# Kernel optimization log

Hardware: AMD Instinct MI355X
Metric: run time of the kernel (lower is better)

Reference implementation:

```python
import jax, jax.numpy as jnp
import numpy as np

B, C = 8, 2048          # batch, out_dim (projection channels)
HG = WG = 32            # global crop feature map
HL = WL = 12            # local crop feature map
STUDENT_TEMP = 0.1
TEMP_SCHEDULE = np.concatenate([np.linspace(0.04, 0.07, 30), np.ones(100 - 30) * 0.07])

# Fixed relative boxes (x1, x2, y1, y2) per (iq, v) crop pair, shared across the
# batch so grid shapes are static. Source computes grid_H from teacher_feat.shape[0]
# (= C, a quirk of the original code) and grid_W from shape[1] (= spatial H); boxes
# are chosen so resulting grids are ~[22-25, 22-24].
PAIRS = [
    (0, 1, (-0.80, 0.70, -0.500, -0.475), (-0.90, 0.60, -0.60, 0.60)),
    (0, 2, (-0.75, 0.75,  0.100,  0.125), (-0.80, 0.80, -0.80, 0.80)),
    (0, 3, (-0.60, 0.90, -0.200, -0.178), (-0.70, 0.90, -0.90, 0.70)),
    (1, 0, (-0.70, 0.80,  0.300,  0.322), (-0.85, 0.65, -0.50, 0.90)),
    (1, 2, (-0.90, 0.50, -0.100, -0.076), (-0.60, 0.95, -0.95, 0.60)),
    (1, 3, (-0.50, 0.95,  0.200,  0.224), (-0.90, 0.90, -0.40, 0.95)),
]


def _grid_dims(box, Hc, Wc):
    x1, x2, y1, y2 = box
    return int(abs(y1 - y2) / 2 * Hc), int(abs(x1 - x2) / 2 * Wc)  # (grid_H, grid_W)


def _make_grid(box, gH, gW):
    # Faithful to source: meshgrid([linspace(y1,y2,gH), linspace(x1,x2,gW)]),
    # stacked so channel 0 holds the y-linspace (which grid_sample reads as x).
    x1, x2, y1, y2 = box
    yy, xx = jnp.meshgrid(jnp.linspace(y1, y2, gH), jnp.linspace(x1, x2, gW), indexing='ij')
    return jnp.stack([yy, xx], axis=-1)  # [gH, gW, 2]


def _grid_sample_border(img, grid):
    # torch.nn.functional.grid_sample, bilinear, padding_mode='border',
    # align_corners=False. img: [B, C, H, W], grid: [gH, gW, 2] (same grid per batch).
    H, W = img.shape[-2], img.shape[-1]
    gx, gy = grid[..., 0], grid[..., 1]
    ix = jnp.clip((gx + 1.0) * (W * 0.5) - 0.5, 0.0, W - 1.0)  # border: clip coords
    iy = jnp.clip((gy + 1.0) * (H * 0.5) - 0.5, 0.0, H - 1.0)
    x0f, y0f = jnp.floor(ix), jnp.floor(iy)
    wx = (ix - x0f)[None, None]  # [1,1,gH,gW]
    wy = (iy - y0f)[None, None]
    x0 = x0f.astype(jnp.int32)
    y0 = y0f.astype(jnp.int32)
    x1 = jnp.minimum(x0 + 1, W - 1)
    y1 = jnp.minimum(y0 + 1, H - 1)
    v00 = img[:, :, y0, x0]
    v01 = img[:, :, y0, x1]
    v10 = img[:, :, y1, x0]
    v11 = img[:, :, y1, x1]
    return (1.0 - wy) * ((1.0 - wx) * v00 + wx * v01) + wy * ((1.0 - wx) * v10 + wx * v11)


def setup_inputs() -> dict:
    key = jax.random.key(0)
    ks = jax.random.split(key, 7)
    return {
        'student_g0': jax.random.normal(ks[0], (B, C, HG, WG), jnp.float32),
        'student_g1': jax.random.normal(ks[1], (B, C, HG, WG), jnp.float32),
        'student_l0': jax.random.normal(ks[2], (B, C, HL, WL), jnp.float32),
        'student_l1': jax.random.normal(ks[3], (B, C, HL, WL), jnp.float32),
        'teacher_g0': jax.random.normal(ks[4], (B, C, HG, WG), jnp.float32),
        'teacher_g1': jax.random.normal(ks[5], (B, C, HG, WG), jnp.float32),
        'center': jax.random.normal(ks[6], (1, C), jnp.float32) * 0.1,
        'epoch': 5,
    }


def reference(student_g0, student_g1, student_l0, student_l1,
              teacher_g0, teacher_g1, center, epoch):
    temp = float(TEMP_SCHEDULE[epoch])
    students = [s / STUDENT_TEMP for s in (student_g0, student_g1, student_l0, student_l1)]
    cen = center[:, :, None, None]  # [1,C,1,1]
    cteach = [jax.nn.softmax((t - cen) / temp, axis=1) for t in (teacher_g0, teacher_g1)]

    losses = []
    for iq, v, tbox, sbox in PAIRS:
        tfeat = cteach[iq]   # [B,C,H,W]
        sfeat = students[v]  # [B,C,h,w]
        # Faithful: source passes (shape[0]=C, shape[1]=spatial H) as (H, W).
        gH, gW = _grid_dims(tbox, C, tfeat.shape[2])
        t_common = jax.lax.stop_gradient(_grid_sample_border(tfeat, _make_grid(tbox, gH, gW)))
        s_common = _grid_sample_border(sfeat, _make_grid(sbox, gH, gW))
        # cross-entropy over channels -> [B, gH, gW]
        loss = (-t_common * jax.nn.log_softmax(s_common, axis=1)).sum(axis=1)
        losses.append(loss.reshape(-1))
    return jnp.concatenate(losses).mean()
```

## Files before the change

kernel.cpp:

```cpp
#include <hip/hip_runtime.h>
#include <hip/hip_fp16.h>

#define NPOS 26688

struct PairInfo {
  int iq, v, Hs, gH, gW, base, per;
  unsigned magicPer, magicW;
  int tOfs, tN, tCb;
  int sN, sCb;
  float tx1, tx2, ty1, ty2;
  float sx1, sx2, sy1, sy2;
};

__constant__ PairInfo g_pairs[6] = {
  {0,1,32,25,24,    0,600, 7158279u,178956971u,    0,2, 7, 22,5, -0.80f,0.70f,-0.500f,-0.475f,  -0.90f,0.60f,-0.60f,0.60f},
  {0,2,12,25,24, 4800,600, 7158279u,178956971u,  512,2,17, 12,0, -0.75f,0.75f, 0.100f, 0.125f,  -0.80f,0.80f,-0.80f,0.80f},
  {0,3,12,22,24, 9600,528, 8134408u,178956971u, 1024,2,12, 12,0, -0.60f,0.90f,-0.200f,-0.178f,  -0.70f,0.90f,-0.90f,0.70f},
  {1,0,32,22,24,13824,528, 8134408u,178956971u, 1536,2,20, 24,7, -0.70f,0.80f, 0.300f, 0.322f,  -0.85f,0.65f,-0.50f,0.90f},
  {1,2,12,24,22,18048,528, 8134408u,195225787u, 2048,3,13, 12,0, -0.90f,0.50f,-0.100f,-0.076f,  -0.60f,0.95f,-0.95f,0.60f},
  {1,3,12,24,23,22272,552, 7780739u,186737709u, 2816,3,18, 12,0, -0.50f,0.95f, 0.200f, 0.224f,  -0.90f,0.90f,-0.40f,0.95f},
};

__constant__ int g_tentX[2][8] = {
  { 7, 8,12,13,17,18,-100,-100},
  {13,14,15,18,19,20,  20,  21},
};
__constant__ int g_tentO[2][8] = {
  {   0,   0,1024,1024, 512, 512,   0,   0},
  {2048,2048,2048,2816,2816,2816,1536,1536},
};
__constant__ int g_tentN[2][8] = {
  {2,2,2,2,2,2,2,2},
  {3,3,3,3,3,3,2,2},
};
__constant__ int g_tentC[2][8] = {
  {0,1,0,1,0,1,0,0},
  {0,1,2,0,1,2,0,1},
};
__constant__ int g_cumTex[6] = {0, 512, 1024, 1536, 2048, 2816};
__constant__ int g_tN[6]    = {2, 2, 2, 2, 3, 3};
__constant__ int g_tCb[6]   = {7, 17, 12, 20, 13, 18};

__device__ inline float get_invtemp(const int* __restrict__ ep) {
  int e = ep[0];
  e = e < 0 ? 0 : (e > 99 ? 99 : e);
  float temp = (e < 30) ? (0.04f + (float)e * (0.03f / 29.0f)) : 0.07f;
  return 1.0f / temp;
}

__device__ inline void lse_merge(float& m, float& s, float m2, float s2) {
  if (m2 > m) { s = s * __expf(m - m2) + s2; m = m2; }
  else s += s2 * __expf(m2 - m);
}

__device__ inline float sel4(const float4& v, int q) {
  return q == 0 ? v.x : q == 1 ? v.y : q == 2 ? v.z : v.w;
}

typedef _Float16 hv2 __attribute__((ext_vector_type(2)));
__device__ inline float fdot2f(__half2 a, __half2 b, float c) {
#if defined(__has_builtin)
#if __has_builtin(__builtin_amdgcn_fdot2)
  return __builtin_amdgcn_fdot2(*reinterpret_cast<hv2*>(&a),
                                *reinterpret_cast<hv2*>(&b), c, false);
#else
  float2 af = __half22float2(a), bf = __half22float2(b);
  return fmaf(af.x, bf.x, fmaf(af.y, bf.y, c));
#endif
#else
  float2 af = __half22float2(a), bf = __half22float2(b);
  return fmaf(af.x, bf.x, fmaf(af.y, bf.y, c));
#endif
}

__global__ __launch_bounds__(256) void dino_stats(
    const float* __restrict__ tg0, const float* __restrict__ tg1,
    const float* __restrict__ cen, const int* __restrict__ ep,
    float* __restrict__ part_m, float* __restrict__ part_s,
    __half* __restrict__ Tc) {
  int bid = blockIdx.x;
  int chunk = bid & 7;
  int y = (bid >> 3) & 31;
  int b = (bid >> 8) & 7;
  int view = bid >> 11;
  const float* __restrict__ src = view ? tg1 : tg0;
  float invtemp = get_invtemp(ep);

  __shared__ float cenl[256];
  __shared__ float pm[32][33], ps[32][33];
  __shared__ float cm[32];
  int t = threadIdx.x;
  cenl[t] = cen[chunk * 256 + t];
  __syncthreads();

  int xg = t & 7, sub = t >> 3;
  const float* sp = src + (((size_t)(b * 2048 + chunk * 256 + sub)) * 32 + y) * 32 + xg * 4;
  float4 lg[8];
#pragma unroll
  for (int k = 0; k < 8; ++k) {
    float4 v = *reinterpret_cast<const float4*>(sp + (size_t)k * 32768);
    float cv = cenl[k * 32 + sub];
    lg[k].x = (v.x - cv) * invtemp;
    lg[k].y = (v.y - cv) * invtemp;
    lg[k].z = (v.z - cv) * invtemp;
    lg[k].w = (v.w - cv) * invtemp;
  }
  float4 mx = lg[0];
#pragma unroll
  for (int k = 1; k < 8; ++k) {
    mx.x = fmaxf(mx.x, lg[k].x); mx.y = fmaxf(mx.y, lg[k].y);
    mx.z = fmaxf(mx.z, lg[k].z); mx.w = fmaxf(mx.w, lg[k].w);
  }
  float4 s = make_float4(0.f, 0.f, 0.f, 0.f);
#pragma unroll
  for (int k = 0; k < 8; ++k) {
    s.x += __expf(lg[k].x - mx.x); s.y += __expf(lg[k].y - mx.y);
    s.z += __expf(lg[k].z - mx.z); s.w += __expf(lg[k].w - mx.w);
  }
  pm[sub][xg * 4 + 0] = mx.x; ps[sub][xg * 4 + 0] = s.x;
  pm[sub][xg * 4 + 1] = mx.y; ps[sub][xg * 4 + 1] = s.y;
  pm[sub][xg * 4 + 2] = mx.z; ps[sub][xg * 4 + 2] = s.z;
  pm[sub][xg * 4 + 3] = mx.w; ps[sub][xg * 4 + 3] = s.w;
  __syncthreads();
  if (t < 32) {
    float M = pm[0][t], S = ps[0][t];
#pragma unroll
    for (int g = 1; g < 32; ++g) lse_merge(M, S, pm[g][t], ps[g][t]);
    part_m[bid * 32 + t] = M;
    part_s[bid * 32 + t] = S;
    cm[t] = M;
  }
  __syncthreads();
  int nent = view ? 8 : 6;
#pragma unroll
  for (int e = 0; e < 8; ++e) {
    if (e < nent) {
      int ex = g_tentX[view][e];
      if ((ex >> 2) == xg) {
        int q = ex & 3;
        float cmx = cm[ex & 31];
        int tex = g_tentO[view][e] + (b * 32 + y) * g_tentN[view][e] + g_tentC[view][e];
        tex = min(max(tex, 0), 3583);
        size_t base = (size_t)tex * 2048 + chunk * 256 + sub;
#pragma unroll
        for (int k = 0; k < 8; ++k)
          Tc[base + k * 32] = __float2half(sel4(lg[k], q) - cmx);
      }
    }
  }
}

__global__ __launch_bounds__(256) void dino_fuse1(
    const float* __restrict__ part_m, const float* __restrict__ part_s,
    float* __restrict__ wm, float* __restrict__ wz,
    const float* __restrict__ sl0, const float* __restrict__ sl1,
    __half* __restrict__ Sl0, __half* __restrict__ Sl1) {
  __shared__ float tile[64 * 145];
  int bid = blockIdx.x;
  int t = threadIdx.x;
  if (bid < 64) {
    int e = bid * 256 + t;
    int x = e & 31;
    int base = (e >> 5) * 8;
    float M = -1e30f, S = 0.f;
#pragma unroll
    for (int c = 0; c < 8; ++c)
      lse_merge(M, S, part_m[(base + c) * 32 + x], part_s[(base + c) * 32 + x]);
    wm[e] = M;
    wz[e] = 1.f / S;
    return;
  }
  int lb = bid - 64;
  int ct = lb & 31;
  int b = (lb >> 5) & 7;
  int vv = lb >> 8;
  const float* __restrict__ src = vv ? sl1 : sl0;
  __half* __restrict__ dst = vv ? Sl1 : Sl0;
  const float* sp = src + ((size_t)(b * 2048 + ct * 64)) * 144;
#pragma unroll
  for (int k = 0; k < 36; ++k) {
    int idx = t + 256 * k;
    int c = idx / 144;
    int yx = idx - c * 144;
    tile[c * 145 + yx] = sp[idx] * 10.f;
  }
  __syncthreads();
  __half* dp = dst + ((size_t)(b * 144)) * 2048 + ct * 64;
#pragma unroll
  for (int k = 0; k < 5; ++k) {
    int idx8 = t + 256 * k;
    if (idx8 < 1152) {
      int yx = idx8 >> 3, q8 = (idx8 & 7) * 8;
      __half hv[8];
#pragma unroll
      for (int j = 0; j < 8; ++j) hv[j] = __float2half(tile[(q8 + j) * 145 + yx]);
      *reinterpret_cast<float4*>(dp + (size_t)yx * 2048 + q8) =
          *reinterpret_cast<float4*>(hv);
    }
  }
}

union H8 { uint4 u; __half2 h[4]; };

__global__ __launch_bounds__(256) void dino_fuse2(
    const __half* __restrict__ Tc, __half* __restrict__ Tp,
    const float* __restrict__ part_m, const float* __restrict__ wm,
    const float* __restrict__ wz,
    const float* __restrict__ sg0, const float* __restrict__ sg1,
    __half* __restrict__ Sg0, __half* __restrict__ Sg1) {
  __shared__ float tile[64][33];
  __shared__ float mk[10];
  int bid = blockIdx.x;
  int t = threadIdx.x;
  if (bid < 3584) {
    int p = 0;
#pragma unroll
    for (int q = 1; q < 6; ++q) p += (bid >= g_cumTex[q]) ? 1 : 0;
    int r = bid - g_cumTex[p];
    int n = g_tN[p];
    int by = (n == 2) ? (r >> 1) : (r / 3);
    by = min(max(by, 0), 255);
    int ci = min(max(r - by * n, 0), n - 1);
    int x = g_tCb[p] + ci;
    int view = (p >= 3) ? 1 : 0;
    int b = by >> 5, y = by & 31;
    int texRow = ((view * 8 + b) * 32 + y);
    if (t < 8) mk[t] = part_m[(texRow * 8 + t) * 32 + x];
    if (t == 8) mk[8] = wm[texRow * 32 + x];
    if (t == 9) mk[9] = wz[texRow * 32 + x];
    __syncthreads();
    int tex = min(g_cumTex[p] + by * n + ci, 3583);
    size_t base = (size_t)tex * 2048 + t * 8;
    H8 hh;
    hh.u = *reinterpret_cast<const uint4*>(Tc + base);
    float off = mk[t >> 5] - mk[8];
    float invS = mk[9];
#pragma unroll
    for (int pc = 0; pc < 4; ++pc) {
      float2 f = __half22float2(hh.h[pc]);
      f.x = __expf(f.x + off) * invS;
      f.y = __expf(f.y + off) * invS;
      hh.h[pc] = __floats2half2_rn(f.x, f.y);
    }
    *reinterpret_cast<uint4*>(Tp + base) = hh.u;
    return;
  }
  int lb = bid - 3584;
  int ct = lb & 31;
  int t2 = lb >> 5;
  int yi = t2 % 26;
  int g = t2 / 26;
  int y = yi + 1;
  int b = g & 7;
  int which = g >> 3;
  const float* __restrict__ src = which ? sg1 : sg0;
  __half* __restrict__ dst = which ? Sg1 : Sg0;
  int cb = which ? 5 : 7;
  int n = which ? 22 : 24;

  int xg = t & 7, ch = t >> 3;
  const float* sp = src + (((size_t)(b * 2048 + ct * 64 + ch)) * 32 + y) * 32 + xg * 4;
  float4 v0 = *reinterpret_cast<const float4*>(sp);
  float4 v1 = *reinterpret_cast<const float4*>(sp + 32768);
  tile[ch][xg * 4 + 0] = v0.x * 10.f;
  tile[ch][xg * 4 + 1] = v0.y * 10.f;
  tile[ch][xg * 4 + 2] = v0.z * 10.f;
  tile[ch][xg * 4 + 3] = v0.w * 10.f;
  tile[ch + 32][xg * 4 + 0] = v1.x * 10.f;
  tile[ch + 32][xg * 4 + 1] = v1.y * 10.f;
  tile[ch + 32][xg * 4 + 2] = v1.z * 10.f;
  tile[ch + 32][xg * 4 + 3] = v1.w * 10.f;
  __syncthreads();
  int xx = t >> 3, ccq = (t & 7) * 8;
  if (xx >= cb && xx < cb + n) {
    __half hv[8];
#pragma unroll
    for (int j = 0; j < 8; ++j) hv[j] = __float2half(tile[ccq + j][xx]);
    __half* dp = dst + ((size_t)((b * 32 + y) * n + (xx - cb))) * 2048 + ct * 64 + ccq;
    *reinterpret_cast<float4*>(dp) = *reinterpret_cast<float4*>(hv);
  }
}

__global__ __launch_bounds__(256) void dino_main(
    const __half* __restrict__ Tp,
    const __half* __restrict__ S0, const __half* __restrict__ S1,
    const __half* __restrict__ S2, const __half* __restrict__ S3,
    float* __restrict__ losses) {
  int wid = threadIdx.x >> 6, lane = threadIdx.x & 63;
  int pair = blockIdx.x / 1200;
  int slot = blockIdx.x - pair * 1200;
  PairInfo pi = g_pairs[pair];
  int posInPair = slot * 4 + wid;
  if (posInPair >= pi.per * 8) return;

  unsigned up = (unsigned)posInPair;
  int b = (int)__umulhi(up, pi.magicPer);
  b = min(max(b, 0), 7);
  int r = posInPair - b * pi.per;
  r = min(max(r, 0), pi.per - 1);
  int i = (int)__umulhi((unsigned)r, pi.magicW);
  i = min(max(i, 0), pi.gH - 1);
  int j = r - i * pi.gW;
  j = min(max(j, 0), pi.gW - 1);

  float tyy = pi.ty1 + (float)i * (pi.ty2 - pi.ty1) / (float)(pi.gH - 1);
  float txx = pi.tx1 + (float)j * (pi.tx2 - pi.tx1) / (float)(pi.gW - 1);
  float tix = fminf(fmaxf((tyy + 1.0f) * 16.0f - 0.5f, 0.0f), 31.0f);
  float tiy = fminf(fmaxf((txx + 1.0f) * 16.0f - 0.5f, 0.0f), 31.0f);
  int tx0 = (int)tix, ty0 = (int)tiy;
  float wxt = tix - (float)tx0, wyt = tiy - (float)ty0;
  int tx1i = min(tx0 + 1, 31), ty1i = min(ty0 + 1, 31);

  int hs = pi.Hs;
  float hh = 0.5f * (float)hs, hm = (float)(hs - 1);
  float syy = pi.sy1 + (float)i * (pi.sy2 - pi.sy1) / (float)(pi.gH - 1);
  float sxx = pi.sx1 + (float)j * (pi.sx2 - pi.sx1) / (float)(pi.gW - 1);
  float six = fminf(fmaxf((syy + 1.0f) * hh - 0.5f, 0.0f), hm);
  float siy = fminf(fmaxf((sxx + 1.0f) * hh - 0.5f, 0.0f), hm);
  int sx0 = (int)six, sy0 = (int)siy;
  float wxs = six - (float)sx0, wys = siy - (float)sy0;
  int sx1i = min(sx0 + 1, hs - 1), sy1i = min(sy0 + 1, hs - 1);

  const __half* __restrict__ S =
      (pi.v == 0) ? S0 : (pi.v == 1) ? S1 : (pi.v == 2) ? S2 : S3;

  int tc0 = min(max(tx0 - pi.tCb, 0), pi.tN - 1);
  int tc1 = min(max(tx1i - pi.tCb, 0), pi.tN - 1);
  int trow = pi.tOfs + (b * 32 + ty0) * pi.tN;
  int trow1 = pi.tOfs + (b * 32 + ty1i) * pi.tN;
  int toff00 = min(trow + tc0, 3583) * 2048;
  int toff01 = min(trow + tc1, 3583) * 2048;
  int toff10 = min(trow1 + tc0, 3583) * 2048;
  int toff11 = min(trow1 + tc1, 3583) * 2048;
  int sc0 = min(max(sx0 - pi.sCb, 0), pi.sN - 1);
  int sc1 = min(max(sx1i - pi.sCb, 0), pi.sN - 1);
  int soff00 = ((b * hs + sy0) * pi.sN + sc0) * 2048;
  int soff01 = ((b * hs + sy0) * pi.sN + sc1) * 2048;
  int soff10 = ((b * hs + sy1i) * pi.sN + sc0) * 2048;
  int soff11 = ((b * hs + sy1i) * pi.sN + sc1) * 2048;

  __half2 wt00 = __float2half2_rn((1.f - wyt) * (1.f - wxt));
  __half2 wt01 = __float2half2_rn((1.f - wyt) * wxt);
  __half2 wt10 = __float2half2_rn(wyt * (1.f - wxt));
  __half2 wt11 = __float2half2_rn(wyt * wxt);
  __half2 ws00 = __float2half2_rn((1.f - wys) * (1.f - wxs));
  __half2 ws01 = __float2half2_rn((1.f - wys) * wxs);
  __half2 ws10 = __float2half2_rn(wys * (1.f - wxs));
  __half2 ws11 = __float2half2_rn(wys * wxs);

  float sum = 0.f, dot = 0.f;
#pragma unroll
  for (int k = 0; k < 4; ++k) {
    int c0 = (k << 9) + (lane << 3);
    H8 t00, t01, t10, t11, a00, a01, a10, a11;
    t00.u = *reinterpret_cast<const uint4*>(Tp + toff00 + c0);
    t01.u = *reinterpret_cast<const uint4*>(Tp + toff01 + c0);
    t10.u = *reinterpret_cast<const uint4*>(Tp + toff10 + c0);
    t11.u = *reinterpret_cast<const uint4*>(Tp + toff11 + c0);
    a00.u = *reinterpret_cast<const uint4*>(S + soff00 + c0);
    a01.u = *reinterpret_cast<const uint4*>(S + soff01 + c0);
    a10.u = *reinterpret_cast<const uint4*>(S + soff10 + c0);
    a11.u = *reinterpret_cast<const uint4*>(S + soff11 + c0);
#pragma unroll
    for (int p = 0; p < 4; ++p) {
      __half2 tc2 = __hmul2(wt00, t00.h[p]);
      tc2 = __hfma2(wt01, t01.h[p], tc2);
      tc2 = __hfma2(wt10, t10.h[p], tc2);
      tc2 = __hfma2(wt11, t11.h[p], tc2);
      __half2 sc2 = __hmul2(ws00, a00.h[p]);
      sc2 = __hfma2(ws01, a01.h[p], sc2);
      sc2 = __hfma2(ws10, a10.h[p], sc2);
      sc2 = __hfma2(ws11, a11.h[p], sc2);
      dot = fdot2f(tc2, sc2, dot);
      float2 scf = __half22float2(sc2);
      sum += __expf(scf.x);
      sum += __expf(scf.y);
    }
  }
#pragma unroll
  for (int off = 32; off; off >>= 1) {
    sum += __shfl_down(sum, off);
    dot += __shfl_down(dot, off);
  }
  if (lane == 0) losses[pi.base + posInPair] = logf(sum) - dot;
}

__global__ __launch_bounds__(1024) void dino_reduce(const float* __restrict__ losses,
                                                    float* __restrict__ out) {
  __shared__ double sd[1024];
  int t = threadIdx.x;
  double a = 0.0;
  for (int i4 = t; i4 < 6672; i4 += 1024) {
    float4 v = *reinterpret_cast<const float4*>(losses + i4 * 4);
    a += (double)v.x + (double)v.y + (double)v.z + (double)v.w;
  }
  sd[t] = a;
  __syncthreads();
  for (int off = 512; off; off >>= 1) {
    if (t < off) sd[t] += sd[t + off];
    __syncthreads();
  }
  if (t == 0) out[0] = (float)(sd[0] / (double)NPOS);
}

extern "C" void kernel_launch(void* const* d_in, const int* in_sizes, int n_in,
                              void* d_out, int out_size, void* d_ws, size_t ws_size,
                              hipStream_t stream) {
  const float* sg0 = (const float*)d_in[0];
  const float* sg1 = (const float*)d_in[1];
  const float* sl0 = (const float*)d_in[2];
  const float* sl1 = (const float*)d_in[3];
  const float* tg0 = (const float*)d_in[4];
  const float* tg1 = (const float*)d_in[5];
  const float* cen = (const float*)d_in[6];
  const int* epoch = (const int*)d_in[7];
  float* out = (float*)d_out;
  char* w = (char*)d_ws;

  const size_t OFF_WM  = 0;
  const size_t OFF_WZ  = 65536;
  const size_t OFF_LOSS= 131072;
  const size_t OFF_PM  = 262144;
  const size_t OFF_PS  = 1310720;
  const size_t OFF_TC  = 2359296;
  const size_t OFF_TP  = 17039360;
  const size_t OFF_SG0 = 31719424;
  const size_t OFF_SG1 = 56885248;
  const size_t OFF_SL0 = 79953920;
  const size_t OFF_SL1 = 84672512;

  float* wm = (float*)(w + OFF_WM);
  float* wz = (float*)(w + OFF_WZ);
  float* losses = (float*)(w + OFF_LOSS);
  float* part_m = (float*)(w + OFF_PM);
  float* part_s = (float*)(w + OFF_PS);
  __half* Tc  = (__half*)(w + OFF_TC);
  __half* Tp  = (__half*)(w + OFF_TP);
  __half* Sg0 = (__half*)(w + OFF_SG0);
  __half* Sg1 = (__half*)(w + OFF_SG1);
  __half* Sl0 = (__half*)(w + OFF_SL0);
  __half* Sl1 = (__half*)(w + OFF_SL1);

  dino_stats<<<8192, 256, 0, stream>>>(tg0, tg1, cen, epoch, part_m, part_s, Tc);
  dino_fuse1<<<576, 256, 0, stream>>>(part_m, part_s, wm, wz, sl0, sl1, Sl0, Sl1);
  dino_fuse2<<<16896, 256, 0, stream>>>(Tc, Tp, part_m, wm, wz, sg0, sg1, Sg0, Sg1);
  dino_main<<<7200, 256, 0, stream>>>(Tp, Sg0, Sg1, Sl0, Sl1, losses);
  dino_reduce<<<1, 1024, 0, stream>>>(losses, out);
}
```

Measured before the change: 134.6 us.

## Fuse teacher stats and student transposes into one kernel, defer LSE merge

Merges the teacher softmax-stats kernel, the local-student transpose and the global-student transpose into a single phase-1 launch. The cross-chunk log-sum-exp merge moves into a separate probability kernel, which removes the wm/wz intermediate buffers and a dependent launch. The per-block 32-way serial LSE merge becomes a two-level tree. The local transpose uses smaller 16-channel tiles with more blocks, so shared-memory footprint drops and more blocks can be resident. In exchange, each probability block recomputes the 8-way merge from the partial statistics.

```diff
diff --git a/kernel.cpp b/kernel.cpp
--- a/kernel.cpp
+++ b/kernel.cpp
@@ -46,11 +46,6 @@
   e = e < 0 ? 0 : (e > 99 ? 99 : e);
   float temp = (e < 30) ? (0.04f + (float)e * (0.03f / 29.0f)) : 0.07f;
   return 1.0f / temp;
-}
-
-__device__ inline void lse_merge(float& m, float& s, float m2, float s2) {
-  if (m2 > m) { s = s * __expf(m - m2) + s2; m = m2; }
-  else s += s2 * __expf(m2 - m);
 }
 
 __device__ inline float sel4(const float4& v, int q) {
@@ -73,179 +68,146 @@
 #endif
 }
 
-__global__ __launch_bounds__(256) void dino_stats(
+__global__ __launch_bounds__(256) void dino_phase1(
     const float* __restrict__ tg0, const float* __restrict__ tg1,
     const float* __restrict__ cen, const int* __restrict__ ep,
     float* __restrict__ part_m, float* __restrict__ part_s,
-    __half* __restrict__ Tc) {
-  int bid = blockIdx.x;
-  int chunk = bid & 7;
-  int y = (bid >> 3) & 31;
-  int b = (bid >> 8) & 7;
-  int view = bid >> 11;
-  const float* __restrict__ src = view ? tg1 : tg0;
-  float invtemp = get_invtemp(ep);
-
-  __shared__ float cenl[256];
-  __shared__ float pm[32][33], ps[32][33];
-  __shared__ float cm[32];
-  int t = threadIdx.x;
-  cenl[t] = cen[chunk * 256 + t];
-  __syncthreads();
-
-  int xg = t & 7, sub = t >> 3;
-  const float* sp = src + (((size_t)(b * 2048 + chunk * 256 + sub)) * 32 + y) * 32 + xg * 4;
-  float4 lg[8];
-#pragma unroll
-  for (int k = 0; k < 8; ++k) {
-    float4 v = *reinterpret_cast<const float4*>(sp + (size_t)k * 32768);
-    float cv = cenl[k * 32 + sub];
-    lg[k].x = (v.x - cv) * invtemp;
-    lg[k].y = (v.y - cv) * invtemp;
-    lg[k].z = (v.z - cv) * invtemp;
-    lg[k].w = (v.w - cv) * invtemp;
-  }
-  float4 mx = lg[0];
-#pragma unroll
-  for (int k = 1; k < 8; ++k) {
-    mx.x = fmaxf(mx.x, lg[k].x); mx.y = fmaxf(mx.y, lg[k].y);
-    mx.z = fmaxf(mx.z, lg[k].z); mx.w = fmaxf(mx.w, lg[k].w);
-  }
-  float4 s = make_float4(0.f, 0.f, 0.f, 0.f);
-#pragma unroll
-  for (int k = 0; k < 8; ++k) {
-    s.x += __expf(lg[k].x - mx.x); s.y += __expf(lg[k].y - mx.y);
-    s.z += __expf(lg[k].z - mx.z); s.w += __expf(lg[k].w - mx.w);
-  }
-  pm[sub][xg * 4 + 0] = mx.x; ps[sub][xg * 4 + 0] = s.x;
-  pm[sub][xg * 4 + 1] = mx.y; ps[sub][xg * 4 + 1] = s.y;
-  pm[sub][xg * 4 + 2] = mx.z; ps[sub][xg * 4 + 2] = s.z;
-  pm[sub][xg * 4 + 3] = mx.w; ps[sub][xg * 4 + 3] = s.w;
-  __syncthreads();
-  if (t < 32) {
-    float M = pm[0][t], S = ps[0][t];
-#pragma unroll
-    for (int g = 1; g < 32; ++g) lse_merge(M, S, pm[g][t], ps[g][t]);
-    part_m[bid * 32 + t] = M;
-    part_s[bid * 32 + t] = S;
-    cm[t] = M;
-  }
-  __syncthreads();
-  int nent = view ? 8 : 6;
-#pragma unroll
-  for (int e = 0; e < 8; ++e) {
-    if (e < nent) {
-      int ex = g_tentX[view][e];
-      if ((ex >> 2) == xg) {
-        int q = ex & 3;
-        float cmx = cm[ex & 31];
-        int tex = g_tentO[view][e] + (b * 32 + y) * g_tentN[view][e] + g_tentC[view][e];
-        tex = min(max(tex, 0), 3583);
-        size_t base = (size_t)tex * 2048 + chunk * 256 + sub;
-#pragma unroll
-        for (int k = 0; k < 8; ++k)
-          Tc[base + k * 32] = __float2half(sel4(lg[k], q) - cmx);
-      }
-    }
-  }
-}
-
-__global__ __launch_bounds__(256) void dino_fuse1(
-    const float* __restrict__ part_m, const float* __restrict__ part_s,
-    float* __restrict__ wm, float* __restrict__ wz,
+    __half* __restrict__ Tc,
     const float* __restrict__ sl0, const float* __restrict__ sl1,
-    __half* __restrict__ Sl0, __half* __restrict__ Sl1) {
-  __shared__ float tile[64 * 145];
+    __half* __restrict__ Sl0, __half* __restrict__ Sl1,
+    const float* __restrict__ sg0, const float* __restrict__ sg1,
+    __half* __restrict__ Sg0, __half* __restrict__ Sg1) {
+  __shared__ float smem[2960];
   int bid = blockIdx.x;
   int t = threadIdx.x;
-  if (bid < 64) {
-    int e = bid * 256 + t;
-    int x = e & 31;
-    int base = (e >> 5) * 8;
-    float M = -1e30f, S = 0.f;
-#pragma unroll
-    for (int c = 0; c < 8; ++c)
-      lse_merge(M, S, part_m[(base + c) * 32 + x], part_s[(base + c) * 32 + x]);
-    wm[e] = M;
-    wz[e] = 1.f / S;
+
+  if (bid < 4096) {
+    int chunk = bid & 7;
+    int y = (bid >> 3) & 31;
+    int b = (bid >> 8) & 7;
+    int view = bid >> 11;
+    const float* __restrict__ src = view ? tg1 : tg0;
+    float invtemp = get_invtemp(ep);
+
+    float* cenl = smem;
+    float* pm   = smem + 256;
+    float* ps   = smem + 1312;
+    float* pm2  = smem + 2368;
+    float* ps2  = smem + 2632;
+    float* cm   = smem + 2896;
+
+    cenl[t] = cen[chunk * 256 + t];
+    __syncthreads();
+
+    int xg = t & 7, sub = t >> 3;
+    const float* sp = src + (((size_t)(b * 2048 + chunk * 256 + sub)) * 32 + y) * 32 + xg * 4;
+    float4 lg[8];
+#pragma unroll
+    for (int k = 0; k < 8; ++k) {
+      float4 v = *reinterpret_cast<const float4*>(sp + (size_t)k * 32768);
+      float cv = cenl[k * 32 + sub];
+      lg[k].x = (v.x - cv) * invtemp;
+      lg[k].y = (v.y - cv) * invtemp;
+      lg[k].z = (v.z - cv) * invtemp;
+      lg[k].w = (v.w - cv) * invtemp;
+    }
+    float4 mx = lg[0];
+#pragma unroll
+    for (int k = 1; k < 8; ++k) {
+      mx.x = fmaxf(mx.x, lg[k].x); mx.y = fmaxf(mx.y, lg[k].y);
+      mx.z = fmaxf(mx.z, lg[k].z); mx.w = fmaxf(mx.w, lg[k].w);
+    }
+    float4 s = make_float4(0.f, 0.f, 0.f, 0.f);
+#pragma unroll
+    for (int k = 0; k < 8; ++k) {
+      s.x += __expf(lg[k].x - mx.x); s.y += __expf(lg[k].y - mx.y);
+      s.z += __expf(lg[k].z - mx.z); s.w += __expf(lg[k].w - mx.w);
+    }
+    pm[sub * 33 + xg * 4 + 0] = mx.x; ps[sub * 33 + xg * 4 + 0] = s.x;
+    pm[sub * 33 + xg * 4 + 1] = mx.y; ps[sub * 33 + xg * 4 + 1] = s.y;
+    pm[sub * 33 + xg * 4 + 2] = mx.z; ps[sub * 33 + xg * 4 + 2] = s.z;
+    pm[sub * 33 + xg * 4 + 3] = mx.w; ps[sub * 33 + xg * 4 + 3] = s.w;
+    __syncthreads();
+    {
+      int x = t & 31, g = t >> 5;
+      float m0 = pm[(g * 4 + 0) * 33 + x], m1 = pm[(g * 4 + 1) * 33 + x];
+      float m2 = pm[(g * 4 + 2) * 33 + x], m3 = pm[(g * 4 + 3) * 33 + x];
+      float M = fmaxf(fmaxf(m0, m1), fmaxf(m2, m3));
+      float S = ps[(g * 4 + 0) * 33 + x] * __expf(m0 - M)
+              + ps[(g * 4 + 1) * 33 + x] * __expf(m1 - M)
+              + ps[(g * 4 + 2) * 33 + x] * __expf(m2 - M)
+              + ps[(g * 4 + 3) * 33 + x] * __expf(m3 - M);
+      pm2[g * 33 + x] = M; ps2[g * 33 + x] = S;
+    }
+    __syncthreads();
+    if (t < 32) {
+      float M = pm2[t];
+#pragma unroll
+      for (int g = 1; g < 8; ++g) M = fmaxf(M, pm2[g * 33 + t]);
+      float S = 0.f;
+#pragma unroll
+      for (int g = 0; g < 8; ++g) S += ps2[g * 33 + t] * __expf(pm2[g * 33 + t] - M);
+      part_m[bid * 32 + t] = M;
+      part_s[bid * 32 + t] = S;
+      cm[t] = M;
+    }
+    __syncthreads();
+    int nent = view ? 8 : 6;
+#pragma unroll
+    for (int e = 0; e < 8; ++e) {
+      if (e < nent) {
+        int ex = g_tentX[view][e];
+        if ((ex >> 2) == xg) {
+          int q = ex & 3;
+          float cmx = cm[ex & 31];
+          int tex = g_tentO[view][e] + (b * 32 + y) * g_tentN[view][e] + g_tentC[view][e];
+          tex = min(max(tex, 0), 3583);
+          size_t base = (size_t)tex * 2048 + chunk * 256 + sub;
+#pragma unroll
+          for (int k = 0; k < 8; ++k)
+            Tc[base + k * 32] = __float2half(sel4(lg[k], q) - cmx);
+        }
+      }
+    }
     return;
   }
-  int lb = bid - 64;
-  int ct = lb & 31;
-  int b = (lb >> 5) & 7;
-  int vv = lb >> 8;
-  const float* __restrict__ src = vv ? sl1 : sl0;
-  __half* __restrict__ dst = vv ? Sl1 : Sl0;
-  const float* sp = src + ((size_t)(b * 2048 + ct * 64)) * 144;
-#pragma unroll
-  for (int k = 0; k < 36; ++k) {
-    int idx = t + 256 * k;
-    int c = idx / 144;
-    int yx = idx - c * 144;
-    tile[c * 145 + yx] = sp[idx] * 10.f;
-  }
-  __syncthreads();
-  __half* dp = dst + ((size_t)(b * 144)) * 2048 + ct * 64;
-#pragma unroll
-  for (int k = 0; k < 5; ++k) {
-    int idx8 = t + 256 * k;
-    if (idx8 < 1152) {
-      int yx = idx8 >> 3, q8 = (idx8 & 7) * 8;
-      __half hv[8];
-#pragma unroll
-      for (int j = 0; j < 8; ++j) hv[j] = __float2half(tile[(q8 + j) * 145 + yx]);
-      *reinterpret_cast<float4*>(dp + (size_t)yx * 2048 + q8) =
-          *reinterpret_cast<float4*>(hv);
-    }
-  }
-}
-
-union H8 { uint4 u; __half2 h[4]; };
-
-__global__ __launch_bounds__(256) void dino_fuse2(
-    const __half* __restrict__ Tc, __half* __restrict__ Tp,
-    const float* __restrict__ part_m, const float* __restrict__ wm,
-    const float* __restrict__ wz,
-    const float* __restrict__ sg0, const float* __restrict__ sg1,
-    __half* __restrict__ Sg0, __half* __restrict__ Sg1) {
-  __shared__ float tile[64][33];
-  __shared__ float mk[10];
-  int bid = blockIdx.x;
-  int t = threadIdx.x;
-  if (bid < 3584) {
-    int p = 0;
-#pragma unroll
-    for (int q = 1; q < 6; ++q) p += (bid >= g_cumTex[q]) ? 1 : 0;
-    int r = bid - g_cumTex[p];
-    int n = g_tN[p];
-    int by = (n == 2) ? (r >> 1) : (r / 3);
-    by = min(max(by, 0), 255);
-    int ci = min(max(r - by * n, 0), n - 1);
-    int x = g_tCb[p] + ci;
-    int view = (p >= 3) ? 1 : 0;
-    int b = by >> 5, y = by & 31;
-    int texRow = ((view * 8 + b) * 32 + y);
-    if (t < 8) mk[t] = part_m[(texRow * 8 + t) * 32 + x];
-    if (t == 8) mk[8] = wm[texRow * 32 + x];
-    if (t == 9) mk[9] = wz[texRow * 32 + x];
-    __syncthreads();
-    int tex = min(g_cumTex[p] + by * n + ci, 3583);
-    size_t base = (size_t)tex * 2048 + t * 8;
-    H8 hh;
-    hh.u = *reinterpret_cast<const uint4*>(Tc + base);
-    float off = mk[t >> 5] - mk[8];
-    float invS = mk[9];
-#pragma unroll
-    for (int pc = 0; pc < 4; ++pc) {
-      float2 f = __half22float2(hh.h[pc]);
-      f.x = __expf(f.x + off) * invS;
-      f.y = __expf(f.y + off) * invS;
-      hh.h[pc] = __floats2half2_rn(f.x, f.y);
-    }
-    *reinterpret_cast<uint4*>(Tp + base) = hh.u;
+
+  if (bid < 6144) {
+    float* tile = smem;
+    int lb = bid - 4096;
+    int ct = lb & 127;
+    int g = lb >> 7;
+    int b = g & 7;
+    int vv = g >> 3;
+    const float* __restrict__ src = vv ? sl1 : sl0;
+    __half* __restrict__ dst = vv ? Sl1 : Sl0;
+    const float* sp = src + ((size_t)(b * 2048 + ct * 16)) * 144;
+#pragma unroll
+    for (int k = 0; k < 9; ++k) {
+      int idx = t + 256 * k;
+      int c = idx / 144;
+      int yx = idx - c * 144;
+      tile[c * 145 + yx] = sp[idx] * 10.f;
+    }
+    __syncthreads();
+    __half* dp = dst + ((size_t)(b * 144)) * 2048 + ct * 16;
+#pragma unroll
+    for (int k = 0; k < 2; ++k) {
+      int u = t + 256 * k;
+      if (u < 288) {
+        int yx = u >> 1, q8 = (u & 1) * 8;
+        __half hv[8];
+#pragma unroll
+        for (int j = 0; j < 8; ++j) hv[j] = __float2half(tile[(q8 + j) * 145 + yx]);
+        *reinterpret_cast<float4*>(dp + (size_t)yx * 2048 + q8) =
+            *reinterpret_cast<float4*>(hv);
+      }
+    }
     return;
   }
-  int lb = bid - 3584;
+
+  float* tile = smem;
+  int lb = bid - 6144;
   int ct = lb & 31;
   int t2 = lb >> 5;
   int yi = t2 % 26;
@@ -262,23 +224,71 @@
   const float* sp = src + (((size_t)(b * 2048 + ct * 64 + ch)) * 32 + y) * 32 + xg * 4;
   float4 v0 = *reinterpret_cast<const float4*>(sp);
   float4 v1 = *reinterpret_cast<const float4*>(sp + 32768);
-  tile[ch][xg * 4 + 0] = v0.x * 10.f;
-  tile[ch][xg * 4 + 1] = v0.y * 10.f;
-  tile[ch][xg * 4 + 2] = v0.z * 10.f;
-  tile[ch][xg * 4 + 3] = v0.w * 10.f;
-  tile[ch + 32][xg * 4 + 0] = v1.x * 10.f;
-  tile[ch + 32][xg * 4 + 1] = v1.y * 10.f;
-  tile[ch + 32][xg * 4 + 2] = v1.z * 10.f;
-  tile[ch + 32][xg * 4 + 3] = v1.w * 10.f;
+  tile[ch * 33 + xg * 4 + 0] = v0.x * 10.f;
+  tile[ch * 33 + xg * 4 + 1] = v0.y * 10.f;
+  tile[ch * 33 + xg * 4 + 2] = v0.z * 10.f;
+  tile[ch * 33 + xg * 4 + 3] = v0.w * 10.f;
+  tile[(ch + 32) * 33 + xg * 4 + 0] = v1.x * 10.f;
+  tile[(ch + 32) * 33 + xg * 4 + 1] = v1.y * 10.f;
+  tile[(ch + 32) * 33 + xg * 4 + 2] = v1.z * 10.f;
+  tile[(ch + 32) * 33 + xg * 4 + 3] = v1.w * 10.f;
   __syncthreads();
   int xx = t >> 3, ccq = (t & 7) * 8;
   if (xx >= cb && xx < cb + n) {
     __half hv[8];
 #pragma unroll
-    for (int j = 0; j < 8; ++j) hv[j] = __float2half(tile[ccq + j][xx]);
+    for (int j = 0; j < 8; ++j) hv[j] = __float2half(tile[(ccq + j) * 33 + xx]);
     __half* dp = dst + ((size_t)((b * 32 + y) * n + (xx - cb))) * 2048 + ct * 64 + ccq;
     *reinterpret_cast<float4*>(dp) = *reinterpret_cast<float4*>(hv);
   }
+}
+
+union H8 { uint4 u; __half2 h[4]; };
+
+__global__ __launch_bounds__(256) void dino_probs(
+    const __half* __restrict__ Tc, __half* __restrict__ Tp,
+    const float* __restrict__ part_m, const float* __restrict__ part_s) {
+  __shared__ float pm8[8], ps8[8];
+  int bid = blockIdx.x;
+  int t = threadIdx.x;
+  int p = 0;
+#pragma unroll
+  for (int q = 1; q < 6; ++q) p += (bid >= g_cumTex[q]) ? 1 : 0;
+  int r = bid - g_cumTex[p];
+  int n = g_tN[p];
+  int by = (n == 2) ? (r >> 1) : (r / 3);
+  by = min(max(by, 0), 255);
+  int ci = min(max(r - by * n, 0), n - 1);
+  int x = g_tCb[p] + ci;
+  int view = (p >= 3) ? 1 : 0;
+  int b = by >> 5, y = by & 31;
+  int texRow = ((view * 8 + b) * 32 + y);
+  if (t < 8) {
+    pm8[t] = part_m[(texRow * 8 + t) * 32 + x];
+    ps8[t] = part_s[(texRow * 8 + t) * 32 + x];
+  }
+  __syncthreads();
+  float M = pm8[0];
+#pragma unroll
+  for (int c = 1; c < 8; ++c) M = fmaxf(M, pm8[c]);
+  float S = 0.f;
+#pragma unroll
+  for (int c = 0; c < 8; ++c) S += ps8[c] * __expf(pm8[c] - M);
+  float invS = 1.f / S;
+  float off = pm8[t >> 5] - M;
+
+  int tex = min(g_cumTex[p] + by * n + ci, 3583);
+  size_t base = (size_t)tex * 2048 + t * 8;
+  H8 hh;
+  hh.u = *reinterpret_cast<const uint4*>(Tc + base);
+#pragma unroll
+  for (int pc = 0; pc < 4; ++pc) {
+    float2 f = __half22float2(hh.h[pc]);
+    f.x = __expf(f.x + off) * invS;
+    f.y = __expf(f.y + off) * invS;
+    hh.h[pc] = __floats2half2_rn(f.x, f.y);
+  }
+  *reinterpret_cast<uint4*>(Tp + base) = hh.u;
 }
 
 __global__ __launch_bounds__(256) void dino_main(
@@ -417,8 +427,6 @@
   float* out = (float*)d_out;
   char* w = (char*)d_ws;
 
-  const size_t OFF_WM  = 0;
-  const size_t OFF_WZ  = 65536;
   const size_t OFF_LOSS= 131072;
   const size_t OFF_PM  = 262144;
   const size_t OFF_PS  = 1310720;
@@ -429,8 +437,6 @@
   const size_t OFF_SL0 = 79953920;
   const size_t OFF_SL1 = 84672512;
 
-  float* wm = (float*)(w + OFF_WM);
-  float* wz = (float*)(w + OFF_WZ);
   float* losses = (float*)(w + OFF_LOSS);
   float* part_m = (float*)(w + OFF_PM);
   float* part_s = (float*)(w + OFF_PS);
@@ -441,9 +447,9 @@
   __half* Sl0 = (__half*)(w + OFF_SL0);
   __half* Sl1 = (__half*)(w + OFF_SL1);
 
-  dino_stats<<<8192, 256, 0, stream>>>(tg0, tg1, cen, epoch, part_m, part_s, Tc);
-  dino_fuse1<<<576, 256, 0, stream>>>(part_m, part_s, wm, wz, sl0, sl1, Sl0, Sl1);
-  dino_fuse2<<<16896, 256, 0, stream>>>(Tc, Tp, part_m, wm, wz, sg0, sg1, Sg0, Sg1);
+  dino_phase1<<<19456, 256, 0, stream>>>(tg0, tg1, cen, epoch, part_m, part_s, Tc,
+                                         sl0, sl1, Sl0, Sl1, sg0, sg1, Sg0, Sg1);
+  dino_probs<<<3584, 256, 0, stream>>>(Tc, Tp, part_m, part_s);
   dino_main<<<7200, 256, 0, stream>>>(Tp, Sg0, Sg1, Sl0, Sl1, losses);
   dino_reduce<<<1, 1024, 0, stream>>>(losses, out);
 }
```

New measurement: 114.0 us (median of 2 runs). 1.18x faster.
